# Kernel optimization log

Measured on AMD Instinct MI355X. Metric: run time of the kernel, lower is better.

## Reference

```python
import jax, jax.numpy as jnp
import numpy as np

EMB = 1024
HEAD = 128

def setup_inputs() -> dict:
    key = jax.random.key(0)
    kx, kk, kq, kv = jax.random.split(key, 4)
    s = 1.0 / np.sqrt(EMB)
    return {
        "x": jax.random.normal(kx, (8, 2048, EMB), dtype=jnp.float32),
        "Wk": jax.random.normal(kk, (EMB, HEAD), dtype=jnp.float32) * s,
        "Wq": jax.random.normal(kq, (EMB, HEAD), dtype=jnp.float32) * s,
        "Wv": jax.random.normal(kv, (EMB, HEAD), dtype=jnp.float32) * s,
    }

def reference(x, Wk, Wq, Wv):
    # x: [B,T,E]; projections (no bias)
    k = jnp.einsum('bte,eh->bth', x, Wk)
    q = jnp.einsum('bte,eh->bth', x, Wq)
    v = jnp.einsum('bte,eh->bth', x, Wv)
    # scores: [B,T,T], NOTE: no 1/sqrt(d) scaling in original module
    qk = jnp.einsum('bih,bjh->bij', q, k)
    T = x.shape[1]
    causal = jnp.tril(jnp.ones((T, T), dtype=bool))  # True = keep
    qk = jnp.where(causal, qk, -jnp.inf)
    # NOTE: softmax over axis -2 (query axis), as in original
    attn = jax.nn.softmax(qk, axis=-2)
    return jnp.einsum('bij,bjh->bih', attn, v)
```

## Files before the change

kernel.cpp:

```cpp
#include <hip/hip_runtime.h>

typedef unsigned short u16;
typedef unsigned int u32;
typedef _Float16 f16;
typedef __attribute__((ext_vector_type(8))) _Float16 f16x8;
typedef __attribute__((ext_vector_type(4))) float f32x4;

constexpr int SEQ = 2048;
constexpr int EMBD = 1024;
constexpr int HD = 128;
constexpr int NB = 8;
constexpr int NSL = 8;

__device__ inline u16 f2h(float f) { return __builtin_bit_cast(u16, (f16)f); }
__device__ inline u32 pack2(float a, float b) { return (u32)f2h(a) | ((u32)f2h(b) << 16); }

__device__ inline f32x4 mfma16(f16x8 a, f16x8 b, f32x4 c) {
  return __builtin_amdgcn_mfma_f32_16x16x32_f16(a, b, c, 0, 0, 0);
}

__device__ __forceinline__ void gload16(const u16* g, u16* l) {
  __builtin_amdgcn_global_load_lds(
      (const __attribute__((address_space(1))) u32*)g,
      (__attribute__((address_space(3))) u32*)l, 16, 0, 0);
}

template<int RB>
__device__ inline f16x8 frag_ld(const u16* lds, int row, int e) {
  int byte = row * RB + ((e * 2) ^ ((row & 7) << 4));
  return *reinterpret_cast<const f16x8*>(reinterpret_cast<const char*>(lds) + byte);
}

__global__ __launch_bounds__(256) void k_cvt_w(const float* __restrict__ Wq,
                                               const float* __restrict__ Wk,
                                               const float* __restrict__ Wv,
                                               u16* __restrict__ Wt) {
  int t = blockIdx.x * 256 + threadIdx.x;
  int e0 = (t & 255) * 4;
  int H = t >> 8;
  int w = H >> 7, h = H & 127;
  const float* W = (w == 0) ? Wq : (w == 1) ? Wk : Wv;
  ushort4 o;
  o.x = f2h(W[(size_t)(e0 + 0) * HD + h]);
  o.y = f2h(W[(size_t)(e0 + 1) * HD + h]);
  o.z = f2h(W[(size_t)(e0 + 2) * HD + h]);
  o.w = f2h(W[(size_t)(e0 + 3) * HD + h]);
  int k0t = e0 >> 6, ec = e0 & 63;
  size_t el = (size_t)(k0t * 384 + H) * 64 + (ec ^ ((H & 7) << 3));
  *reinterpret_cast<ushort4*>(Wt + el) = o;
}

__global__ __launch_bounds__(512, 4) void k_proj(const float* __restrict__ x,
                                                 const u16* __restrict__ Wt,
                                                 u16* __restrict__ Qb,
                                                 u16* __restrict__ Kb,
                                                 u16* __restrict__ Vtb) {
  __shared__ __align__(16) u16 As[2][64 * 64];
  __shared__ __align__(16) u16 Bs[2][192 * 64];
  const int mt = blockIdx.x, ny = blockIdx.y;
  const int t = threadIdx.x, lane = t & 63, wave = t >> 6;
  const int rh = (wave & 1) * 32, cq = (wave >> 1) * 48;
  const int ar = t >> 3, ac = t & 7;
  const float* asrc = x + (size_t)(mt * 64 + ar) * EMBD + ac * 8;
  const int adst = ar * 64 + ((ac * 8) ^ ((ar & 7) << 3));
  f32x4 zero = {0.f, 0.f, 0.f, 0.f};
  f32x4 acc[2][3];
#pragma unroll
  for (int a = 0; a < 2; ++a)
#pragma unroll
    for (int b = 0; b < 3; ++b) acc[a][b] = zero;

  {
#pragma unroll
    for (int q = 0; q < 3; ++q) {
      int lin = q * 512 + t;
      gload16(Wt + ny * 12288 + lin * 8, &Bs[0][lin * 8]);
    }
    float4 a0 = *reinterpret_cast<const float4*>(asrc);
    float4 a1 = *reinterpret_cast<const float4*>(asrc + 4);
    uint4 o = {pack2(a0.x, a0.y), pack2(a0.z, a0.w), pack2(a1.x, a1.y), pack2(a1.z, a1.w)};
    *reinterpret_cast<uint4*>(&As[0][adst]) = o;
  }
  __syncthreads();
  int cur = 0;
  for (int s = 0; s < 16; ++s) {
    float4 a0, a1;
    const bool pf = (s < 15);
    if (pf) {
#pragma unroll
      for (int q = 0; q < 3; ++q) {
        int lin = q * 512 + t;
        gload16(Wt + (s + 1) * 24576 + ny * 12288 + lin * 8, &Bs[cur ^ 1][lin * 8]);
      }
      a0 = *reinterpret_cast<const float4*>(asrc + (s + 1) * 64);
      a1 = *reinterpret_cast<const float4*>(asrc + (s + 1) * 64 + 4);
    }
#pragma unroll
    for (int kk = 0; kk < 2; ++kk) {
      f16x8 af0 = frag_ld<128>(As[cur], rh + (lane & 15), kk * 32 + (lane >> 4) * 8);
      f16x8 af1 = frag_ld<128>(As[cur], rh + 16 + (lane & 15), kk * 32 + (lane >> 4) * 8);
#pragma unroll
      for (int fc = 0; fc < 3; ++fc) {
        f16x8 bw = frag_ld<128>(Bs[cur], cq + fc * 16 + (lane & 15), kk * 32 + (lane >> 4) * 8);
        acc[0][fc] = mfma16(af0, bw, acc[0][fc]);
        acc[1][fc] = mfma16(af1, bw, acc[1][fc]);
      }
    }
    if (pf) {
      uint4 o = {pack2(a0.x, a0.y), pack2(a0.z, a0.w), pack2(a1.x, a1.y), pack2(a1.z, a1.w)};
      *reinterpret_cast<uint4*>(&As[cur ^ 1][adst]) = o;
    }
    __syncthreads();
    cur ^= 1;
  }
#pragma unroll
  for (int fi = 0; fi < 2; ++fi)
#pragma unroll
    for (int fc = 0; fc < 3; ++fc) {
      int gcol = ny * 192 + cq + fc * 16 + (lane & 15);
      int w = gcol >> 7, h = gcol & 127;
      int i0 = mt * 64 + rh + fi * 16 + (lane >> 4) * 4;
      if (w < 2) {
        u16* P = w ? Kb : Qb;
#pragma unroll
        for (int r = 0; r < 4; ++r) {
          int i = i0 + r;
          P[(size_t)i * 128 + (h ^ ((i & 7) << 3))] = f2h(acc[fi][fc][r]);
        }
      } else {
        int bb = i0 >> 11, jt = (i0 >> 6) & 31, tl = i0 & 63;
        ushort4 o = {f2h(acc[fi][fc][0]), f2h(acc[fi][fc][1]),
                     f2h(acc[fi][fc][2]), f2h(acc[fi][fc][3])};
        size_t el = ((size_t)(bb * 32 + jt) * 128 + h) * 64 + (tl ^ ((h & 7) << 3));
        *reinterpret_cast<ushort4*>(Vtb + el) = o;
      }
    }
}

__device__ inline void merge_ml(float& m, float& l, float m2, float l2) {
  float mn = fmaxf(m, m2);
  float a = (m > -1e37f) ? l * __expf(m - mn) : 0.f;
  float b = (m2 > -1e37f) ? l2 * __expf(m2 - mn) : 0.f;
  m = mn;
  l = a + b;
}

__global__ __launch_bounds__(256, 2) void k_statsA(const u16* __restrict__ Qb,
                                                   const u16* __restrict__ Kb,
                                                   float* __restrict__ mpart,
                                                   float* __restrict__ lpart) {
  __shared__ __align__(16) u16 Qs[2][128 * 128];
  const int id = blockIdx.y * 64 + blockIdx.x;
  const int bb = id & 7, z = (id >> 3) & 7, sl = id >> 6;
  const int t = threadIdx.x, lane = t & 63, wj = (t >> 6) * 32;
  f32x4 zero = {0.f, 0.f, 0.f, 0.f};

  for (int ph = 0; ph < 2; ++ph) {
    const int jt = ph ? 15 - z : z;
    __syncthreads();
#pragma unroll
    for (int q = 0; q < 8; ++q) {
      int lin = q * 256 + t;
      gload16(Kb + ((size_t)bb * SEQ + jt * 128) * 128 + lin * 8, &Qs[0][lin * 8]);
    }
    __syncthreads();
    f16x8 af[2][4];
#pragma unroll
    for (int fj = 0; fj < 2; ++fj)
#pragma unroll
      for (int kk = 0; kk < 4; ++kk)
        af[fj][kk] = frag_ld<256>(Qs[0], wj + fj * 16 + (lane & 15), kk * 32 + (lane >> 4) * 8);
    float m[2][4], l[2][4];
#pragma unroll
    for (int a = 0; a < 2; ++a)
#pragma unroll
      for (int r = 0; r < 4; ++r) {
        m[a][r] = -INFINITY;
        l[a][r] = 0.f;
      }
    const int it0 = jt + ((sl - jt) & 7);
    int cur = 1;
    if (it0 < 16) {
#pragma unroll
      for (int q = 0; q < 8; ++q) {
        int lin = q * 256 + t;
        gload16(Qb + ((size_t)bb * SEQ + it0 * 128) * 128 + lin * 8, &Qs[1][lin * 8]);
      }
      for (int it = it0; it < 16; it += 8) {
        __syncthreads();
        if (it + 8 < 16) {
#pragma unroll
          for (int q = 0; q < 8; ++q) {
            int lin = q * 256 + t;
            gload16(Qb + ((size_t)bb * SEQ + (it + 8) * 128) * 128 + lin * 8,
                    &Qs[cur ^ 1][lin * 8]);
          }
        }
        f32x4 acc[2][8];
#pragma unroll
        for (int a = 0; a < 2; ++a)
#pragma unroll
          for (int b = 0; b < 8; ++b) acc[a][b] = zero;
        __builtin_amdgcn_s_setprio(1);
#pragma unroll
        for (int kk = 0; kk < 4; ++kk)
#pragma unroll
          for (int fi = 0; fi < 8; ++fi) {
            f16x8 bq = frag_ld<256>(Qs[cur], fi * 16 + (lane & 15), kk * 32 + (lane >> 4) * 8);
            acc[0][fi] = mfma16(af[0][kk], bq, acc[0][fi]);
            acc[1][fi] = mfma16(af[1][kk], bq, acc[1][fi]);
          }
        __builtin_amdgcn_s_setprio(0);
#pragma unroll
        for (int fj = 0; fj < 2; ++fj)
#pragma unroll
          for (int r = 0; r < 4; ++r) {
            int jg = jt * 128 + wj + fj * 16 + (lane >> 4) * 4 + r;
            float v[8];
            float vmax = -INFINITY;
#pragma unroll
            for (int fi = 0; fi < 8; ++fi) {
              int ig = it * 128 + fi * 16 + (lane & 15);
              v[fi] = (ig >= jg) ? acc[fj][fi][r] : -INFINITY;
              vmax = fmaxf(vmax, v[fi]);
            }
            if (vmax > -1e37f) {
              float mn = fmaxf(m[fj][r], vmax);
              float sc = (m[fj][r] > -1e37f) ? __expf(m[fj][r] - mn) : 0.f;
              float ss = 0.f;
#pragma unroll
              for (int fi = 0; fi < 8; ++fi)
                ss += (v[fi] > -1e37f) ? __expf(v[fi] - mn) : 0.f;
              l[fj][r] = l[fj][r] * sc + ss;
              m[fj][r] = mn;
            }
          }
        cur ^= 1;
      }
    }
#pragma unroll
    for (int fj = 0; fj < 2; ++fj)
#pragma unroll
      for (int r = 0; r < 4; ++r)
        for (int msk = 1; msk <= 8; msk <<= 1) {
          float m2 = __shfl_xor(m[fj][r], msk);
          float l2 = __shfl_xor(l[fj][r], msk);
          merge_ml(m[fj][r], l[fj][r], m2, l2);
        }
    if ((lane & 15) == 0) {
#pragma unroll
      for (int fj = 0; fj < 2; ++fj)
#pragma unroll
        for (int r = 0; r < 4; ++r) {
          int j = jt * 128 + wj + fj * 16 + (lane >> 4) * 4 + r;
          size_t idx = (size_t)sl * (NB * SEQ) + (size_t)bb * SEQ + j;
          mpart[idx] = m[fj][r];
          lpart[idx] = l[fj][r];
        }
    }
  }
}

__global__ __launch_bounds__(256) void k_stats_reduce(const float* __restrict__ mpart,
                                                      const float* __restrict__ lpart,
                                                      float* __restrict__ Cg) {
  int idx = blockIdx.x * 256 + threadIdx.x;
  float m = -INFINITY;
#pragma unroll
  for (int sl = 0; sl < NSL; sl++) m = fmaxf(m, mpart[sl * (NB * SEQ) + idx]);
  float l = 0.f;
#pragma unroll
  for (int sl = 0; sl < NSL; sl++) {
    float ms = mpart[sl * (NB * SEQ) + idx];
    if (ms > -1e37f) l += lpart[sl * (NB * SEQ) + idx] * __expf(ms - m);
  }
  Cg[idx] = m + __logf(l);
}

__global__ __launch_bounds__(256, 2) void k_passB(const u16* __restrict__ Qb,
                                                  const u16* __restrict__ Kb,
                                                  const u16* __restrict__ Vtb,
                                                  const float* __restrict__ Cg,
                                                  u16* __restrict__ opart) {
  __shared__ __align__(16) u16 Ks2[2][64 * 128];
  __shared__ __align__(16) u16 Vs2[2][128 * 64];
  __shared__ __align__(16) u16 Ps[128 * 64];
  const int id = blockIdx.y * 64 + blockIdx.x;
  const int bb = id & 7, z = (id >> 3) & 7, sl = id >> 6;
  const int t = threadIdx.x, lane = t & 63, wi = (t >> 6) * 32;
  f32x4 zero = {0.f, 0.f, 0.f, 0.f};

  auto stageKV = [&](int jt, int b) {
#pragma unroll
    for (int q = 0; q < 4; ++q) {
      int lin = q * 256 + t;
      gload16(Kb + ((size_t)bb * SEQ + jt * 64) * 128 + lin * 8, &Ks2[b][lin * 8]);
    }
#pragma unroll
    for (int q = 0; q < 4; ++q) {
      int lin = q * 256 + t;
      gload16(Vtb + ((size_t)bb * 32 + jt) * 8192 + lin * 8, &Vs2[b][lin * 8]);
    }
  };

  for (int ph = 0; ph < 2; ++ph) {
    const int it = ph ? 15 - z : z;
    f16x8 qf[2][4];
#pragma unroll
    for (int fi = 0; fi < 2; ++fi)
#pragma unroll
      for (int kk = 0; kk < 4; ++kk) {
        size_t gi = (size_t)bb * SEQ + it * 128 + wi + fi * 16 + (lane & 15);
        int e0 = kk * 32 + (lane >> 4) * 8;
        qf[fi][kk] = *reinterpret_cast<const f16x8*>(Qb + gi * 128 + (e0 ^ (((int)gi & 7) << 3)));
      }
    f32x4 accO[2][8];
#pragma unroll
    for (int a = 0; a < 2; ++a)
#pragma unroll
      for (int b = 0; b < 8; ++b) accO[a][b] = zero;
    const int jtmax = 2 * it + 1;
    __syncthreads();
    if (sl <= jtmax) stageKV(sl, 0);
    int cur = 0;
    for (int jt = sl; jt <= jtmax; jt += 8) {
      __syncthreads();
      if (jt + 8 <= jtmax) stageKV(jt + 8, cur ^ 1);
      float cj[4];
#pragma unroll
      for (int fj = 0; fj < 4; ++fj)
        cj[fj] = Cg[bb * SEQ + jt * 64 + fj * 16 + (lane & 15)];
      f32x4 accS[2][4];
#pragma unroll
      for (int a = 0; a < 2; ++a)
#pragma unroll
        for (int b = 0; b < 4; ++b) accS[a][b] = zero;
      __builtin_amdgcn_s_setprio(1);
#pragma unroll
      for (int kk = 0; kk < 4; ++kk)
#pragma unroll
        for (int fj = 0; fj < 4; ++fj) {
          f16x8 bk = frag_ld<256>(Ks2[cur], fj * 16 + (lane & 15), kk * 32 + (lane >> 4) * 8);
          accS[0][fj] = mfma16(qf[0][kk], bk, accS[0][fj]);
          accS[1][fj] = mfma16(qf[1][kk], bk, accS[1][fj]);
        }
      __builtin_amdgcn_s_setprio(0);
#pragma unroll
      for (int fj = 0; fj < 4; ++fj) {
        int jloc = fj * 16 + (lane & 15);
        int jg = jt * 64 + jloc;
        float c = cj[fj];
#pragma unroll
        for (int fi = 0; fi < 2; ++fi)
#pragma unroll
          for (int r = 0; r < 4; ++r) {
            int iloc = wi + fi * 16 + (lane >> 4) * 4 + r;
            int ig = it * 128 + iloc;
            float p = __expf(accS[fi][fj][r] - c);
            if (ig < jg) p = 0.f;
            Ps[iloc * 64 + (jloc ^ ((iloc & 7) << 3))] = f2h(p);
          }
      }
      __builtin_amdgcn_s_setprio(1);
#pragma unroll
      for (int ks = 0; ks < 2; ++ks) {
        f16x8 pa0 = frag_ld<128>(Ps, wi + (lane & 15), ks * 32 + (lane >> 4) * 8);
        f16x8 pa1 = frag_ld<128>(Ps, wi + 16 + (lane & 15), ks * 32 + (lane >> 4) * 8);
#pragma unroll
        for (int fh = 0; fh < 8; ++fh) {
          f16x8 bv = frag_ld<128>(Vs2[cur], fh * 16 + (lane & 15), ks * 32 + (lane >> 4) * 8);
          accO[0][fh] = mfma16(pa0, bv, accO[0][fh]);
          accO[1][fh] = mfma16(pa1, bv, accO[1][fh]);
        }
      }
      __builtin_amdgcn_s_setprio(0);
      cur ^= 1;
    }
#pragma unroll
    for (int fi = 0; fi < 2; ++fi)
#pragma unroll
      for (int fh = 0; fh < 8; ++fh)
#pragma unroll
        for (int r = 0; r < 4; ++r) {
          int ig = it * 128 + wi + fi * 16 + (lane >> 4) * 4 + r;
          int h = fh * 16 + (lane & 15);
          opart[(((size_t)sl * NB + bb) * SEQ + ig) * HD + h] = f2h(accO[fi][fh][r]);
        }
  }
}

__global__ __launch_bounds__(256) void k_reduceB(const u16* __restrict__ opart,
                                                 float* __restrict__ out) {
  size_t base = ((size_t)blockIdx.x * 256 + threadIdx.x) * 8;
  const size_t S = (size_t)NB * SEQ * HD;
  float s[8];
#pragma unroll
  for (int j = 0; j < 8; j++) s[j] = 0.f;
#pragma unroll
  for (int sl = 0; sl < NSL; sl++) {
    f16x8 v = *reinterpret_cast<const f16x8*>(opart + sl * S + base);
#pragma unroll
    for (int j = 0; j < 8; j++) s[j] += (float)v[j];
  }
  float4 o0 = {s[0], s[1], s[2], s[3]};
  float4 o1 = {s[4], s[5], s[6], s[7]};
  *reinterpret_cast<float4*>(out + base) = o0;
  *reinterpret_cast<float4*>(out + base + 4) = o1;
}

extern "C" void kernel_launch(void* const* d_in, const int* in_sizes, int n_in,
                              void* d_out, int out_size, void* d_ws, size_t ws_size,
                              hipStream_t stream) {
  (void)in_sizes; (void)n_in; (void)out_size; (void)ws_size;
  const float* x = (const float*)d_in[0];
  const float* Wk = (const float*)d_in[1];
  const float* Wq = (const float*)d_in[2];
  const float* Wv = (const float*)d_in[3];
  float* out = (float*)d_out;
  char* ws = (char*)d_ws;

  u16* Wt = (u16*)(ws + 0);
  u16* Qb = (u16*)(ws + 786432);
  u16* Kb = (u16*)(ws + 4980736);
  u16* Vtb = (u16*)(ws + 9175040);
  float* mpart = (float*)(ws + 13369344);
  float* lpart = (float*)(ws + 13893632);
  float* Cg = (float*)(ws + 14417920);
  u16* opart = (u16*)(ws + 14548992);

  k_cvt_w<<<384, 256, 0, stream>>>(Wq, Wk, Wv, Wt);
  k_proj<<<dim3(256, 2), 512, 0, stream>>>(x, Wt, Qb, Kb, Vtb);
  k_statsA<<<dim3(64, 8), 256, 0, stream>>>(Qb, Kb, mpart, lpart);
  k_stats_reduce<<<64, 256, 0, stream>>>(mpart, lpart, Cg);
  k_passB<<<dim3(64, 8), 256, 0, stream>>>(Qb, Kb, Vtb, Cg, opart);
  k_reduceB<<<1024, 256, 0, stream>>>(opart, out);
}
```

Measured before the change: 83.82 us.

## Retile passB to 64-row query tiles with 4 splits, deepen projection prefetch, skip masking off-diagonal

```diff
diff --git a/kernel.cpp b/kernel.cpp
--- a/kernel.cpp
+++ b/kernel.cpp
@@ -10,7 +10,8 @@
 constexpr int EMBD = 1024;
 constexpr int HD = 128;
 constexpr int NB = 8;
-constexpr int NSL = 8;
+constexpr int NSLS = 8;
+constexpr int NSLP = 4;
 
 __device__ inline u16 f2h(float f) { return __builtin_bit_cast(u16, (f16)f); }
 __device__ inline u32 pack2(float a, float b) { return (u32)f2h(a) | ((u32)f2h(b) << 16); }
@@ -70,31 +71,41 @@
 #pragma unroll
     for (int b = 0; b < 3; ++b) acc[a][b] = zero;
 
+  float4 xe0, xe1, xo0, xo1;
+  xe0 = *reinterpret_cast<const float4*>(asrc);
+  xe1 = *reinterpret_cast<const float4*>(asrc + 4);
+#pragma unroll
+  for (int q = 0; q < 3; ++q) {
+    int lin = q * 512 + t;
+    gload16(Wt + ny * 12288 + lin * 8, &Bs[0][lin * 8]);
+  }
   {
-#pragma unroll
-    for (int q = 0; q < 3; ++q) {
-      int lin = q * 512 + t;
-      gload16(Wt + ny * 12288 + lin * 8, &Bs[0][lin * 8]);
-    }
-    float4 a0 = *reinterpret_cast<const float4*>(asrc);
-    float4 a1 = *reinterpret_cast<const float4*>(asrc + 4);
-    uint4 o = {pack2(a0.x, a0.y), pack2(a0.z, a0.w), pack2(a1.x, a1.y), pack2(a1.z, a1.w)};
+    uint4 o = {pack2(xe0.x, xe0.y), pack2(xe0.z, xe0.w), pack2(xe1.x, xe1.y), pack2(xe1.z, xe1.w)};
     *reinterpret_cast<uint4*>(&As[0][adst]) = o;
   }
+  xo0 = *reinterpret_cast<const float4*>(asrc + 64);
+  xo1 = *reinterpret_cast<const float4*>(asrc + 68);
   __syncthreads();
-  int cur = 0;
+#pragma unroll 2
   for (int s = 0; s < 16; ++s) {
-    float4 a0, a1;
-    const bool pf = (s < 15);
-    if (pf) {
+    const int cur = s & 1;
+    if (s + 1 < 16) {
 #pragma unroll
       for (int q = 0; q < 3; ++q) {
         int lin = q * 512 + t;
         gload16(Wt + (s + 1) * 24576 + ny * 12288 + lin * 8, &Bs[cur ^ 1][lin * 8]);
       }
-      a0 = *reinterpret_cast<const float4*>(asrc + (s + 1) * 64);
-      a1 = *reinterpret_cast<const float4*>(asrc + (s + 1) * 64 + 4);
-    }
+    }
+    if (s + 2 < 16) {
+      if (cur == 0) {
+        xe0 = *reinterpret_cast<const float4*>(asrc + (s + 2) * 64);
+        xe1 = *reinterpret_cast<const float4*>(asrc + (s + 2) * 64 + 4);
+      } else {
+        xo0 = *reinterpret_cast<const float4*>(asrc + (s + 2) * 64);
+        xo1 = *reinterpret_cast<const float4*>(asrc + (s + 2) * 64 + 4);
+      }
+    }
+    __builtin_amdgcn_s_setprio(1);
 #pragma unroll
     for (int kk = 0; kk < 2; ++kk) {
       f16x8 af0 = frag_ld<128>(As[cur], rh + (lane & 15), kk * 32 + (lane >> 4) * 8);
@@ -106,12 +117,16 @@
         acc[1][fc] = mfma16(af1, bw, acc[1][fc]);
       }
     }
-    if (pf) {
-      uint4 o = {pack2(a0.x, a0.y), pack2(a0.z, a0.w), pack2(a1.x, a1.y), pack2(a1.z, a1.w)};
+    __builtin_amdgcn_s_setprio(0);
+    if (s + 1 < 16) {
+      uint4 o;
+      if (cur == 0)
+        o = {pack2(xo0.x, xo0.y), pack2(xo0.z, xo0.w), pack2(xo1.x, xo1.y), pack2(xo1.z, xo1.w)};
+      else
+        o = {pack2(xe0.x, xe0.y), pack2(xe0.z, xe0.w), pack2(xe1.x, xe1.y), pack2(xe1.z, xe1.w)};
       *reinterpret_cast<uint4*>(&As[cur ^ 1][adst]) = o;
     }
     __syncthreads();
-    cur ^= 1;
   }
 #pragma unroll
   for (int fi = 0; fi < 2; ++fi)
@@ -211,30 +226,48 @@
             acc[1][fi] = mfma16(af[1][kk], bq, acc[1][fi]);
           }
         __builtin_amdgcn_s_setprio(0);
-#pragma unroll
-        for (int fj = 0; fj < 2; ++fj)
-#pragma unroll
-          for (int r = 0; r < 4; ++r) {
-            int jg = jt * 128 + wj + fj * 16 + (lane >> 4) * 4 + r;
-            float v[8];
-            float vmax = -INFINITY;
-#pragma unroll
-            for (int fi = 0; fi < 8; ++fi) {
-              int ig = it * 128 + fi * 16 + (lane & 15);
-              v[fi] = (ig >= jg) ? acc[fj][fi][r] : -INFINITY;
-              vmax = fmaxf(vmax, v[fi]);
+        if (it == jt) {
+#pragma unroll
+          for (int fj = 0; fj < 2; ++fj)
+#pragma unroll
+            for (int r = 0; r < 4; ++r) {
+              int jg = jt * 128 + wj + fj * 16 + (lane >> 4) * 4 + r;
+              float v[8];
+              float vmax = -INFINITY;
+#pragma unroll
+              for (int fi = 0; fi < 8; ++fi) {
+                int ig = it * 128 + fi * 16 + (lane & 15);
+                v[fi] = (ig >= jg) ? acc[fj][fi][r] : -INFINITY;
+                vmax = fmaxf(vmax, v[fi]);
+              }
+              if (vmax > -1e37f) {
+                float mn = fmaxf(m[fj][r], vmax);
+                float sc = (m[fj][r] > -1e37f) ? __expf(m[fj][r] - mn) : 0.f;
+                float ss = 0.f;
+#pragma unroll
+                for (int fi = 0; fi < 8; ++fi)
+                  ss += (v[fi] > -1e37f) ? __expf(v[fi] - mn) : 0.f;
+                l[fj][r] = l[fj][r] * sc + ss;
+                m[fj][r] = mn;
+              }
             }
-            if (vmax > -1e37f) {
+        } else {
+#pragma unroll
+          for (int fj = 0; fj < 2; ++fj)
+#pragma unroll
+            for (int r = 0; r < 4; ++r) {
+              float vmax = acc[fj][0][r];
+#pragma unroll
+              for (int fi = 1; fi < 8; ++fi) vmax = fmaxf(vmax, acc[fj][fi][r]);
               float mn = fmaxf(m[fj][r], vmax);
-              float sc = (m[fj][r] > -1e37f) ? __expf(m[fj][r] - mn) : 0.f;
+              float sc = __expf(m[fj][r] - mn);
               float ss = 0.f;
 #pragma unroll
-              for (int fi = 0; fi < 8; ++fi)
-                ss += (v[fi] > -1e37f) ? __expf(v[fi] - mn) : 0.f;
+              for (int fi = 0; fi < 8; ++fi) ss += __expf(acc[fj][fi][r] - mn);
               l[fj][r] = l[fj][r] * sc + ss;
               m[fj][r] = mn;
             }
-          }
+        }
         cur ^= 1;
       }
     }
@@ -267,10 +300,10 @@
   int idx = blockIdx.x * 256 + threadIdx.x;
   float m = -INFINITY;
 #pragma unroll
-  for (int sl = 0; sl < NSL; sl++) m = fmaxf(m, mpart[sl * (NB * SEQ) + idx]);
+  for (int sl = 0; sl < NSLS; sl++) m = fmaxf(m, mpart[sl * (NB * SEQ) + idx]);
   float l = 0.f;
 #pragma unroll
-  for (int sl = 0; sl < NSL; sl++) {
+  for (int sl = 0; sl < NSLS; sl++) {
     float ms = mpart[sl * (NB * SEQ) + idx];
     if (ms > -1e37f) l += lpart[sl * (NB * SEQ) + idx] * __expf(ms - m);
   }
@@ -284,10 +317,10 @@
                                                   u16* __restrict__ opart) {
   __shared__ __align__(16) u16 Ks2[2][64 * 128];
   __shared__ __align__(16) u16 Vs2[2][128 * 64];
-  __shared__ __align__(16) u16 Ps[128 * 64];
+  __shared__ __align__(16) u16 Ps[64 * 64];
   const int id = blockIdx.y * 64 + blockIdx.x;
-  const int bb = id & 7, z = (id >> 3) & 7, sl = id >> 6;
-  const int t = threadIdx.x, lane = t & 63, wi = (t >> 6) * 32;
+  const int bb = id & 7, zp = (id >> 3) & 15, sl = id >> 7;
+  const int t = threadIdx.x, lane = t & 63, wave = t >> 6;
   f32x4 zero = {0.f, 0.f, 0.f, 0.f};
 
   auto stageKV = [&](int jt, int b) {
@@ -304,45 +337,37 @@
   };
 
   for (int ph = 0; ph < 2; ++ph) {
-    const int it = ph ? 15 - z : z;
-    f16x8 qf[2][4];
-#pragma unroll
-    for (int fi = 0; fi < 2; ++fi)
-#pragma unroll
-      for (int kk = 0; kk < 4; ++kk) {
-        size_t gi = (size_t)bb * SEQ + it * 128 + wi + fi * 16 + (lane & 15);
-        int e0 = kk * 32 + (lane >> 4) * 8;
-        qf[fi][kk] = *reinterpret_cast<const f16x8*>(Qb + gi * 128 + (e0 ^ (((int)gi & 7) << 3)));
-      }
-    f32x4 accO[2][8];
-#pragma unroll
-    for (int a = 0; a < 2; ++a)
-#pragma unroll
-      for (int b = 0; b < 8; ++b) accO[a][b] = zero;
-    const int jtmax = 2 * it + 1;
+    const int it = ph ? 31 - zp : zp;
+    f16x8 qf[4];
+#pragma unroll
+    for (int kk = 0; kk < 4; ++kk) {
+      size_t gi = (size_t)bb * SEQ + it * 64 + wave * 16 + (lane & 15);
+      int e0 = kk * 32 + (lane >> 4) * 8;
+      qf[kk] = *reinterpret_cast<const f16x8*>(Qb + gi * 128 + (e0 ^ (((int)gi & 7) << 3)));
+    }
+    f32x4 accO[8];
+#pragma unroll
+    for (int b = 0; b < 8; ++b) accO[b] = zero;
     __syncthreads();
-    if (sl <= jtmax) stageKV(sl, 0);
+    if (sl <= it) stageKV(sl, 0);
     int cur = 0;
-    for (int jt = sl; jt <= jtmax; jt += 8) {
+    for (int jt = sl; jt <= it; jt += NSLP) {
       __syncthreads();
-      if (jt + 8 <= jtmax) stageKV(jt + 8, cur ^ 1);
+      if (jt + NSLP <= it) stageKV(jt + NSLP, cur ^ 1);
       float cj[4];
 #pragma unroll
       for (int fj = 0; fj < 4; ++fj)
         cj[fj] = Cg[bb * SEQ + jt * 64 + fj * 16 + (lane & 15)];
-      f32x4 accS[2][4];
-#pragma unroll
-      for (int a = 0; a < 2; ++a)
-#pragma unroll
-        for (int b = 0; b < 4; ++b) accS[a][b] = zero;
+      f32x4 accS[4];
+#pragma unroll
+      for (int b = 0; b < 4; ++b) accS[b] = zero;
       __builtin_amdgcn_s_setprio(1);
 #pragma unroll
       for (int kk = 0; kk < 4; ++kk)
 #pragma unroll
         for (int fj = 0; fj < 4; ++fj) {
           f16x8 bk = frag_ld<256>(Ks2[cur], fj * 16 + (lane & 15), kk * 32 + (lane >> 4) * 8);
-          accS[0][fj] = mfma16(qf[0][kk], bk, accS[0][fj]);
-          accS[1][fj] = mfma16(qf[1][kk], bk, accS[1][fj]);
+          accS[fj] = mfma16(qf[kk], bk, accS[fj]);
         }
       __builtin_amdgcn_s_setprio(0);
 #pragma unroll
@@ -351,41 +376,35 @@
         int jg = jt * 64 + jloc;
         float c = cj[fj];
 #pragma unroll
-        for (int fi = 0; fi < 2; ++fi)
-#pragma unroll
-          for (int r = 0; r < 4; ++r) {
-            int iloc = wi + fi * 16 + (lane >> 4) * 4 + r;
-            int ig = it * 128 + iloc;
-            float p = __expf(accS[fi][fj][r] - c);
-            if (ig < jg) p = 0.f;
-            Ps[iloc * 64 + (jloc ^ ((iloc & 7) << 3))] = f2h(p);
-          }
+        for (int r = 0; r < 4; ++r) {
+          int iloc = wave * 16 + (lane >> 4) * 4 + r;
+          int ig = it * 64 + iloc;
+          float p = __expf(accS[fj][r] - c);
+          if (ig < jg) p = 0.f;
+          Ps[iloc * 64 + (jloc ^ ((iloc & 7) << 3))] = f2h(p);
+        }
       }
       __builtin_amdgcn_s_setprio(1);
 #pragma unroll
       for (int ks = 0; ks < 2; ++ks) {
-        f16x8 pa0 = frag_ld<128>(Ps, wi + (lane & 15), ks * 32 + (lane >> 4) * 8);
-        f16x8 pa1 = frag_ld<128>(Ps, wi + 16 + (lane & 15), ks * 32 + (lane >> 4) * 8);
+        f16x8 pa = frag_ld<128>(Ps, wave * 16 + (lane & 15), ks * 32 + (lane >> 4) * 8);
 #pragma unroll
         for (int fh = 0; fh < 8; ++fh) {
           f16x8 bv = frag_ld<128>(Vs2[cur], fh * 16 + (lane & 15), ks * 32 + (lane >> 4) * 8);
-          accO[0][fh] = mfma16(pa0, bv, accO[0][fh]);
-          accO[1][fh] = mfma16(pa1, bv, accO[1][fh]);
+          accO[fh] = mfma16(pa, bv, accO[fh]);
         }
       }
       __builtin_amdgcn_s_setprio(0);
       cur ^= 1;
     }
 #pragma unroll
-    for (int fi = 0; fi < 2; ++fi)
-#pragma unroll
-      for (int fh = 0; fh < 8; ++fh)
-#pragma unroll
-        for (int r = 0; r < 4; ++r) {
-          int ig = it * 128 + wi + fi * 16 + (lane >> 4) * 4 + r;
-          int h = fh * 16 + (lane & 15);
-          opart[(((size_t)sl * NB + bb) * SEQ + ig) * HD + h] = f2h(accO[fi][fh][r]);
-        }
+    for (int fh = 0; fh < 8; ++fh)
+#pragma unroll
+      for (int r = 0; r < 4; ++r) {
+        int ig = it * 64 + wave * 16 + (lane >> 4) * 4 + r;
+        int h = fh * 16 + (lane & 15);
+        opart[(((size_t)sl * NB + bb) * SEQ + ig) * HD + h] = f2h(accO[fh][r]);
+      }
   }
 }
 
@@ -397,7 +416,7 @@
 #pragma unroll
   for (int j = 0; j < 8; j++) s[j] = 0.f;
 #pragma unroll
-  for (int sl = 0; sl < NSL; sl++) {
+  for (int sl = 0; sl < NSLP; sl++) {
     f16x8 v = *reinterpret_cast<const f16x8*>(opart + sl * S + base);
 #pragma unroll
     for (int j = 0; j < 8; j++) s[j] += (float)v[j];
@@ -426,7 +445,7 @@
   float* mpart = (float*)(ws + 13369344);
   float* lpart = (float*)(ws + 13893632);
   float* Cg = (float*)(ws + 14417920);
-  u16* opart = (u16*)(ws + 14548992);
+  u16* opart = (u16*)(ws + 14483456);
 
   k_cvt_w<<<384, 256, 0, stream>>>(Wq, Wk, Wv, Wt);
   k_proj<<<dim3(256, 2), 512, 0, stream>>>(x, Wt, Qb, Kb, Vtb);
```

Result: faster. 79.15 us (-5.6%).
